# Performance work log

Hardware: AMD Instinct MI355X
Metric: run time of the kernel (lower is better)

## Reference

```python
import jax, jax.numpy as jnp
import numpy as np

D = 1024
N_HEADS = 16
HEAD_DIM = D // N_HEADS
EPS = 1e-09


def setup_inputs() -> dict:
    key = jax.random.key(0)
    ks = jax.random.split(key, 8)
    s = 0.02
    return {
        "x": jax.random.normal(ks[0], (2, 2048, D), jnp.float32),
        "Wq": jax.random.normal(ks[1], (D, D), jnp.float32) * s,
        "Wk": jax.random.normal(ks[2], (D, D), jnp.float32) * s,
        "Wv": jax.random.normal(ks[3], (D, D), jnp.float32) * s,
        "Wo": jax.random.normal(ks[4], (D, D), jnp.float32) * s,
        "W_up": jax.random.normal(ks[5], (4 * D, D), jnp.float32) * s,
        "W_down": jax.random.normal(ks[6], (D, 4 * D), jnp.float32) * s,
        "ln1_mean_scale": jnp.zeros((D,), jnp.float32),
        "ln1_std_scale": jnp.ones((D,), jnp.float32),
        "ln2_mean_scale": jnp.zeros((D,), jnp.float32),
        "ln2_std_scale": jnp.ones((D,), jnp.float32),
    }


def _ln(x, mean_scale, std_scale):
    mean = jnp.mean(x, axis=-1, keepdims=True)
    # torch .var() defaults to unbiased (ddof=1)
    std = jnp.sqrt(jnp.var(x, axis=-1, keepdims=True, ddof=1) + EPS)
    return (x - mean) / std * std_scale + mean_scale


def _attention(x, Wq, Wk, Wv, Wo):
    B, S, _ = x.shape
    # nn.Linear(bias=False): y = x @ W.T
    def heads(W):
        return (x @ W.T).reshape(B, S, N_HEADS, HEAD_DIM).transpose(0, 2, 1, 3)
    Q, K, V = heads(Wq), heads(Wk), heads(Wv)
    scale = jnp.sqrt(jnp.asarray(HEAD_DIM, Q.dtype))
    logits = jnp.einsum('bhqd,bhkd->bhqk', Q, K) / scale  # [B,H,S,S]
    causal = jnp.tril(jnp.ones((S, S), bool))
    logits = jnp.where(causal, logits, -jnp.inf)
    A = jax.nn.softmax(logits, axis=-1)
    preout = jnp.einsum('bhqk,bhkd->bhqd', A, V)  # [B,H,S,hd]
    # Wo.weight.T reshaped to (n_heads, d_head, d_model); per-head out then sum
    W_O = Wo.T.reshape(N_HEADS, HEAD_DIM, D)
    return jnp.einsum('bhsd,hdm->bsm', preout, W_O)


def _mlp(x, W_up, W_down):
    mid = jax.nn.gelu(x @ W_up.T, approximate=False)
    return mid @ W_down.T


def reference(x, Wq, Wk, Wv, Wo, W_up, W_down,
              ln1_mean_scale, ln1_std_scale, ln2_mean_scale, ln2_std_scale):
    x = x + _attention(_ln(x, ln1_mean_scale, ln1_std_scale), Wq, Wk, Wv, Wo)
    x = x + _mlp(_ln(x, ln2_mean_scale, ln2_std_scale), W_up, W_down)
    return x
```

## Files before the change

### kernel.cpp

```cpp
#include <hip/hip_runtime.h>
#include <hip/hip_bf16.h>
#include <cstdint>
#include <cstddef>

#define D_MODEL 1024
#define SEQ     2048
#define NTOK    4096
#define NH      16
#define HD      64

typedef __attribute__((ext_vector_type(8))) short sh8;
typedef __attribute__((ext_vector_type(4))) float f32x4;

#define GLL(g, s) __builtin_amdgcn_global_load_lds(                                   \
    (const __attribute__((address_space(1))) void*)(g),                               \
    (__attribute__((address_space(3))) void*)(s), 16, 0, 0)

__device__ __forceinline__ unsigned short f2b(float f) {
  union { float f; unsigned u; } v; v.f = f;
  unsigned r = v.u + 0x7FFFu + ((v.u >> 16) & 1u);
  return (unsigned short)(r >> 16);
}
__device__ __forceinline__ float b2f(unsigned short h) {
  union { unsigned u; float f; } v; v.u = ((unsigned)h) << 16;
  return v.f;
}

__global__ __launch_bounds__(256) void cast6_kernel(
    const float* __restrict__ q, const float* __restrict__ k, const float* __restrict__ v,
    const float* __restrict__ o, const float* __restrict__ u, const float* __restrict__ d,
    unsigned short* __restrict__ oq, unsigned short* __restrict__ ok,
    unsigned short* __restrict__ ov, unsigned short* __restrict__ oo,
    unsigned short* __restrict__ ou, unsigned short* __restrict__ od) {
  int bid = blockIdx.x;
  const float* src; unsigned short* dst; int base;
  if      (bid < 1024) { src = q; dst = oq; base = bid; }
  else if (bid < 2048) { src = k; dst = ok; base = bid - 1024; }
  else if (bid < 3072) { src = v; dst = ov; base = bid - 2048; }
  else if (bid < 4096) { src = o; dst = oo; base = bid - 3072; }
  else if (bid < 8192) { src = u; dst = ou; base = bid - 4096; }
  else                 { src = d; dst = od; base = bid - 8192; }
  int i = base * 1024 + threadIdx.x * 4;
  float4 vv = *(const float4*)(src + i);
  ushort4 w;
  w.x = f2b(vv.x); w.y = f2b(vv.y); w.z = f2b(vv.z); w.w = f2b(vv.w);
  *(ushort4*)(dst + i) = w;
}

__global__ __launch_bounds__(256) void ln_kernel(const float* __restrict__ x,
                                                 const float* __restrict__ msc,
                                                 const float* __restrict__ ssc,
                                                 unsigned short* __restrict__ out) {
  const int t = blockIdx.x;
  const int tid = threadIdx.x;
  const float4 v = ((const float4*)(x + (size_t)t * D_MODEL))[tid];
  float s = v.x + v.y + v.z + v.w;
  float q = v.x * v.x + v.y * v.y + v.z * v.z + v.w * v.w;
  #pragma unroll
  for (int off = 32; off; off >>= 1) {
    s += __shfl_xor(s, off);
    q += __shfl_xor(q, off);
  }
  __shared__ float sh[8];
  const int w = tid >> 6;
  if ((tid & 63) == 0) { sh[w * 2] = s; sh[w * 2 + 1] = q; }
  __syncthreads();
  s = sh[0] + sh[2] + sh[4] + sh[6];
  q = sh[1] + sh[3] + sh[5] + sh[7];
  const float mean = s * (1.0f / D_MODEL);
  const float var = (q - (float)D_MODEL * mean * mean) * (1.0f / (D_MODEL - 1));
  const float rstd = rsqrtf(var + 1e-9f);
  const float4 ms = ((const float4*)msc)[tid];
  const float4 ss = ((const float4*)ssc)[tid];
  ushort4 o;
  o.x = f2b((v.x - mean) * rstd * ss.x + ms.x);
  o.y = f2b((v.y - mean) * rstd * ss.y + ms.y);
  o.z = f2b((v.z - mean) * rstd * ss.z + ms.z);
  o.w = f2b((v.w - mean) * rstd * ss.w + ms.w);
  ((ushort4*)(out + (size_t)t * D_MODEL))[tid] = o;
}

template <bool WITH_X>
__global__ __launch_bounds__(256) void reduce2_kernel(const unsigned short* __restrict__ p0,
                                                      const unsigned short* __restrict__ p1,
                                                      const float* __restrict__ x,
                                                      float* __restrict__ out) {
  int i = (blockIdx.x * 256 + threadIdx.x) * 4;
  ushort4 a = *(const ushort4*)(p0 + i);
  ushort4 b = *(const ushort4*)(p1 + i);
  float4 base = WITH_X ? *(const float4*)(x + i) : *(const float4*)(out + i);
  float4 r;
  r.x = base.x + b2f(a.x) + b2f(b.x);
  r.y = base.y + b2f(a.y) + b2f(b.y);
  r.z = base.z + b2f(a.z) + b2f(b.z);
  r.w = base.w + b2f(a.w) + b2f(b.w);
  *(float4*)(out + i) = r;
}

__global__ __launch_bounds__(256) void vtrans_kernel(const unsigned short* __restrict__ qkv,
                                                     unsigned short* __restrict__ vt) {
  __shared__ unsigned short T[64][72];
  const int st = blockIdx.x;
  const int b  = blockIdx.y >> 4;
  const int dt = blockIdx.y & 15;
  const int tid = threadIdx.x;
  const int s0 = st * 64, d0 = dt * 64;
  const int r = tid >> 2, c0 = (tid & 3) * 16;
  const unsigned short* src = qkv + ((size_t)b * SEQ + s0 + r) * 3072 + 2 * D_MODEL + d0 + c0;
  *(uint4*)&T[r][c0]     = *(const uint4*)(src);
  *(uint4*)&T[r][c0 + 8] = *(const uint4*)(src + 8);
  __syncthreads();
  unsigned short buf[16] __attribute__((aligned(16)));
  #pragma unroll
  for (int j = 0; j < 16; j++) buf[j] = T[c0 + j][r];
  unsigned short* dst = vt + ((size_t)b * D_MODEL + d0 + r) * SEQ + s0 + c0;
  *(uint4*)(dst)     = *(uint4*)&buf[0];
  *(uint4*)(dst + 8) = *(uint4*)&buf[8];
}

template <int EP>
__global__ __launch_bounds__(256) void gemm_nt(const unsigned short* __restrict__ A,
                                               const unsigned short* __restrict__ B,
                                               int N, int LD, int Kext,
                                               unsigned short* __restrict__ Cbf,
                                               unsigned short* __restrict__ Cbf2) {
  __shared__ __align__(16) unsigned short As[128 * 64];
  __shared__ __align__(16) unsigned short Bs[128 * 64];
  const int tid = threadIdx.x;
  const int w = tid >> 6, l = tid & 63, ln = tid & 15, quad = (tid & 63) >> 4;
  const int wr = (w >> 1) * 64, wc = (w & 1) * 64;
  const int m0 = blockIdx.y * 128, n0 = blockIdx.x * 128;
  const int koff = blockIdx.z * Kext;

  const int sr = l >> 3, sc = l & 7;
  const unsigned short* AgS = A + (size_t)(m0 + w * 32 + sr) * LD + koff + ((sc ^ sr) * 8);
  const unsigned short* BgS = B + (size_t)(n0 + w * 32 + sr) * LD + koff + ((sc ^ sr) * 8);
  unsigned short* AsW = &As[(w * 32) * 64];
  unsigned short* BsW = &Bs[(w * 32) * 64];

  f32x4 acc[4][4] = {};

  for (int k0 = 0; k0 < Kext; k0 += 64) {
    __syncthreads();
    #pragma unroll
    for (int off = 0; off < 32; off += 8) {
      GLL(AgS + k0 + (size_t)off * LD, AsW + off * 64);
      GLL(BgS + k0 + (size_t)off * LD, BsW + off * 64);
    }
    __syncthreads();
    sh8 af[2][4], bfr[2][4];
    #pragma unroll
    for (int kk = 0; kk < 2; kk++) {
      #pragma unroll
      for (int i = 0; i < 4; i++)
        af[kk][i]  = *(const sh8*)&As[(wr + i * 16 + ln) * 64 + (((kk * 4 + quad) ^ (ln & 7)) * 8)];
      #pragma unroll
      for (int j = 0; j < 4; j++)
        bfr[kk][j] = *(const sh8*)&Bs[(wc + j * 16 + ln) * 64 + (((kk * 4 + quad) ^ (ln & 7)) * 8)];
    }
    #pragma unroll
    for (int kk = 0; kk < 2; kk++)
      #pragma unroll
      for (int i = 0; i < 4; i++)
        #pragma unroll
        for (int j = 0; j < 4; j++)
          acc[i][j] = __builtin_amdgcn_mfma_f32_16x16x32_bf16(af[kk][i], bfr[kk][j], acc[i][j], 0, 0, 0);
  }

  unsigned short* C = blockIdx.z ? Cbf2 : Cbf;
  #pragma unroll
  for (int i = 0; i < 4; i++) {
    #pragma unroll
    for (int rr = 0; rr < 4; rr++) {
      const int gm = m0 + wr + i * 16 + quad * 4 + rr;
      #pragma unroll
      for (int j = 0; j < 4; j++) {
        const int gn = n0 + wc + j * 16 + ln;
        const float v = acc[i][j][rr];
        const size_t idx = (size_t)gm * N + gn;
        if (EP == 0) {
          C[idx] = f2b(v);
        } else {
          const float g = 0.5f * v * (1.0f + erff(v * 0.70710678118654752f));
          C[idx] = f2b(g);
        }
      }
    }
  }
}

__global__ __launch_bounds__(256) void attn_kernel(const unsigned short* __restrict__ qkv,
                                                   const unsigned short* __restrict__ vt,
                                                   unsigned short* __restrict__ outp) {
  const int qt = (SEQ / 64 - 1) - blockIdx.x;
  const int bh = blockIdx.y;
  const int b = bh >> 4, h = bh & 15;
  const int tid = threadIdx.x;
  const int w = tid >> 6, l = tid & 63, ln = tid & 15, quad = (tid & 63) >> 4;
  const int q0 = qt * 64;

  __shared__ __align__(16) unsigned short Ks[64 * 64];
  __shared__ __align__(16) unsigned short Vs[64 * 64];
  __shared__ __align__(16) unsigned short Ps[4][16 * 72];

  const size_t rstride = 3 * D_MODEL;
  const unsigned short* Qg = qkv + (size_t)b * SEQ * rstride + h * HD;
  const unsigned short* Kg = Qg + D_MODEL;
  const unsigned short* Vg = vt + ((size_t)b * D_MODEL + h * HD) * SEQ;

  sh8 qf[2];
  {
    const unsigned short* qrow = Qg + (size_t)(q0 + w * 16 + ln) * rstride + quad * 8;
    qf[0] = *(const sh8*)(qrow);
    qf[1] = *(const sh8*)(qrow + 32);
  }

  const int lr3 = l >> 3, lp3 = l & 7;
  const int cS = (lp3 ^ lr3) * 8;
  const unsigned short* KgS = Kg + (size_t)(w * 16 + lr3) * rstride + cS;
  unsigned short* KsW = &Ks[(w * 16) * 64];
  const unsigned short* VgS = Vg + (size_t)(w * 16 + lr3) * SEQ + cS;
  unsigned short* VsW = &Vs[(w * 16) * 64];
  unsigned short* Psw = &Ps[w][0];

  f32x4 o[4] = {};
  float lpart[4] = {0.f, 0.f, 0.f, 0.f};
  const int rbase = q0 + w * 16 + quad * 4;

  auto tile = [&](int kt, bool diag) {
    __syncthreads();
    GLL(KgS + (size_t)(kt * 64) * rstride,     KsW);
    GLL(KgS + (size_t)(kt * 64 + 8) * rstride, KsW + 8 * 64);
    GLL(VgS + kt * 64,           VsW);
    GLL(VgS + 8 * SEQ + kt * 64, VsW + 8 * 64);
    __syncthreads();

    #pragma unroll
    for (int ct = 0; ct < 4; ct++) {
      const int k = ct * 16 + ln;
      f32x4 z = {};
      z = __builtin_amdgcn_mfma_f32_16x16x32_bf16(
          qf[0], *(const sh8*)&Ks[k * 64 + ((quad ^ (k & 7)) * 8)], z, 0, 0, 0);
      z = __builtin_amdgcn_mfma_f32_16x16x32_bf16(
          qf[1], *(const sh8*)&Ks[k * 64 + (((4 + quad) ^ (k & 7)) * 8)], z, 0, 0, 0);
      const int cg = kt * 64 + ct * 16 + ln;
      #pragma unroll
      for (int rr = 0; rr < 4; rr++) {
        float e = exp2f(fmaf(z[rr], 0.18033688011112042f, -5.770780163555853f));
        if (diag && cg > rbase + rr) e = 0.0f;
        lpart[rr] += e;
        Psw[(quad * 4 + rr) * 72 + ct * 16 + ln] = f2b(e);
      }
    }

    #pragma unroll
    for (int kk = 0; kk < 2; kk++) {
      sh8 pf = *(const sh8*)&Psw[ln * 72 + kk * 32 + quad * 8];
      #pragma unroll
      for (int c2 = 0; c2 < 4; c2++) {
        const int d = c2 * 16 + ln;
        sh8 vf = *(const sh8*)&Vs[d * 64 + ((((kk * 4 + quad) ^ (d & 7))) * 8)];
        o[c2] = __builtin_amdgcn_mfma_f32_16x16x32_bf16(pf, vf, o[c2], 0, 0, 0);
      }
    }
  };

  for (int kt = 0; kt < qt; kt++) tile(kt, false);
  tile(qt, true);

  #pragma unroll
  for (int rr = 0; rr < 4; rr++) {
    #pragma unroll
    for (int off = 1; off < 16; off <<= 1) lpart[rr] += __shfl_xor(lpart[rr], off);
  }

  #pragma unroll
  for (int rr = 0; rr < 4; rr++) {
    const int row = q0 + w * 16 + quad * 4 + rr;
    const float inv = 1.0f / lpart[rr];
    const size_t base = ((size_t)b * SEQ + row) * D_MODEL + h * HD;
    #pragma unroll
    for (int c2 = 0; c2 < 4; c2++)
      outp[base + c2 * 16 + ln] = f2b(o[c2][rr] * inv);
  }
}

extern "C" void kernel_launch(void* const* d_in, const int* in_sizes, int n_in,
                              void* d_out, int out_size, void* d_ws, size_t ws_size,
                              hipStream_t stream) {
  const float* x    = (const float*)d_in[0];
  const float* Wq   = (const float*)d_in[1];
  const float* Wk   = (const float*)d_in[2];
  const float* Wv   = (const float*)d_in[3];
  const float* Wo   = (const float*)d_in[4];
  const float* Wup  = (const float*)d_in[5];
  const float* Wdn  = (const float*)d_in[6];
  const float* ln1m = (const float*)d_in[7];
  const float* ln1s = (const float*)d_in[8];
  const float* ln2m = (const float*)d_in[9];
  const float* ln2s = (const float*)d_in[10];
  float* out = (float*)d_out;

  unsigned short* ws = (unsigned short*)d_ws;
  size_t off = 0;
  unsigned short* wqkv = ws + off; off += (size_t)3072 * 1024;
  unsigned short* wo   = ws + off; off += (size_t)1024 * 1024;
  unsigned short* wup  = ws + off; off += (size_t)4096 * 1024;
  unsigned short* wdn  = ws + off; off += (size_t)1024 * 4096;
  unsigned short* xln  = ws + off; off += (size_t)NTOK * 1024;
  unsigned short* qkvb = ws + off; off += (size_t)NTOK * 3072;
  unsigned short* pre  = ws + off; off += (size_t)NTOK * 1024;
  unsigned short* mid  = qkvb;
  unsigned short* vtg  = xln;
  unsigned short* po0  = qkvb;
  unsigned short* po1  = qkvb + (size_t)NTOK * 1024;
  unsigned short* pd0  = ws;
  unsigned short* pd1  = xln;

  cast6_kernel<<<12288, 256, 0, stream>>>(Wq, Wk, Wv, Wo, Wup, Wdn,
      wqkv, wqkv + (size_t)1024 * 1024, wqkv + (size_t)2 * 1024 * 1024, wo, wup, wdn);

  ln_kernel<<<NTOK, 256, 0, stream>>>(x, ln1m, ln1s, xln);
  gemm_nt<0><<<dim3(24, 32, 1), 256, 0, stream>>>(xln, wqkv, 3072, 1024, 1024, qkvb, nullptr);
  vtrans_kernel<<<dim3(32, 32), 256, 0, stream>>>(qkvb, vtg);
  attn_kernel<<<dim3(SEQ / 64, 2 * NH), 256, 0, stream>>>(qkvb, vtg, pre);
  gemm_nt<0><<<dim3(8, 32, 2), 256, 0, stream>>>(pre, wo, 1024, 1024, 512, po0, po1);
  reduce2_kernel<true><<<4096, 256, 0, stream>>>(po0, po1, x, out);
  ln_kernel<<<NTOK, 256, 0, stream>>>(out, ln2m, ln2s, xln);
  gemm_nt<2><<<dim3(32, 32, 1), 256, 0, stream>>>(xln, wup, 4096, 1024, 1024, mid, nullptr);
  gemm_nt<0><<<dim3(8, 32, 2), 256, 0, stream>>>(mid, wdn, 1024, 4096, 2048, pd0, pd1);
  reduce2_kernel<false><<<4096, 256, 0, stream>>>(pd0, pd1, nullptr, out);
}
```

Baseline: 373.3 us.

## Split attention key range across two blocks and combine partial outputs

The causal attention kernel now launches two blocks per query tile. Each block handles alternating key tiles and writes unnormalized bf16 partial outputs plus partial row sums. A new combine kernel adds the two partials and divides by the summed denominators. This doubles the grid and shortens the longest per-block causal loop, which should improve load balance and occupancy. The cost is an extra kernel launch, extra partial-output traffic, and bf16 rounding of unnormalized values, using the output buffer and the dead QKV weight region as scratch.

```diff
diff --git a/kernel.cpp b/kernel.cpp
--- a/kernel.cpp
+++ b/kernel.cpp
@@ -97,6 +97,24 @@
   *(float4*)(out + i) = r;
 }
 
+__global__ __launch_bounds__(256) void attn_combine_kernel(
+    unsigned short* __restrict__ p0, const unsigned short* __restrict__ p1,
+    const float* __restrict__ l0, const float* __restrict__ l1) {
+  int i = (blockIdx.x * 256 + threadIdx.x) * 4;
+  const int tok = i >> 10, ch = i & 1023;
+  const int b = tok >> 11, s = tok & 2047, h = ch >> 6;
+  const int lidx = ((b << 4) + h) * 2048 + s;
+  const float inv = 1.0f / (l0[lidx] + l1[lidx]);
+  ushort4 a = *(const ushort4*)(p0 + i);
+  ushort4 c = *(const ushort4*)(p1 + i);
+  ushort4 r;
+  r.x = f2b((b2f(a.x) + b2f(c.x)) * inv);
+  r.y = f2b((b2f(a.y) + b2f(c.y)) * inv);
+  r.z = f2b((b2f(a.z) + b2f(c.z)) * inv);
+  r.w = f2b((b2f(a.w) + b2f(c.w)) * inv);
+  *(ushort4*)(p0 + i) = r;
+}
+
 __global__ __launch_bounds__(256) void vtrans_kernel(const unsigned short* __restrict__ qkv,
                                                      unsigned short* __restrict__ vt) {
   __shared__ unsigned short T[64][72];
@@ -191,8 +209,12 @@
 
 __global__ __launch_bounds__(256) void attn_kernel(const unsigned short* __restrict__ qkv,
                                                    const unsigned short* __restrict__ vt,
-                                                   unsigned short* __restrict__ outp) {
+                                                   unsigned short* __restrict__ p0,
+                                                   unsigned short* __restrict__ p1,
+                                                   float* __restrict__ l0,
+                                                   float* __restrict__ l1) {
   const int qt = (SEQ / 64 - 1) - blockIdx.x;
+  const int z  = blockIdx.z;
   const int bh = blockIdx.y;
   const int b = bh >> 4, h = bh & 15;
   const int tid = threadIdx.x;
@@ -238,15 +260,15 @@
     #pragma unroll
     for (int ct = 0; ct < 4; ct++) {
       const int k = ct * 16 + ln;
-      f32x4 z = {};
-      z = __builtin_amdgcn_mfma_f32_16x16x32_bf16(
-          qf[0], *(const sh8*)&Ks[k * 64 + ((quad ^ (k & 7)) * 8)], z, 0, 0, 0);
-      z = __builtin_amdgcn_mfma_f32_16x16x32_bf16(
-          qf[1], *(const sh8*)&Ks[k * 64 + (((4 + quad) ^ (k & 7)) * 8)], z, 0, 0, 0);
+      f32x4 zz = {};
+      zz = __builtin_amdgcn_mfma_f32_16x16x32_bf16(
+          qf[0], *(const sh8*)&Ks[k * 64 + ((quad ^ (k & 7)) * 8)], zz, 0, 0, 0);
+      zz = __builtin_amdgcn_mfma_f32_16x16x32_bf16(
+          qf[1], *(const sh8*)&Ks[k * 64 + (((4 + quad) ^ (k & 7)) * 8)], zz, 0, 0, 0);
       const int cg = kt * 64 + ct * 16 + ln;
       #pragma unroll
       for (int rr = 0; rr < 4; rr++) {
-        float e = exp2f(fmaf(z[rr], 0.18033688011112042f, -5.770780163555853f));
+        float e = exp2f(fmaf(zz[rr], 0.18033688011112042f, -5.770780163555853f));
         if (diag && cg > rbase + rr) e = 0.0f;
         lpart[rr] += e;
         Psw[(quad * 4 + rr) * 72 + ct * 16 + ln] = f2b(e);
@@ -265,8 +287,8 @@
     }
   };
 
-  for (int kt = 0; kt < qt; kt++) tile(kt, false);
-  tile(qt, true);
+  for (int kt = z; kt < qt; kt += 2) tile(kt, false);
+  if ((qt & 1) == z) tile(qt, true);
 
   #pragma unroll
   for (int rr = 0; rr < 4; rr++) {
@@ -274,14 +296,20 @@
     for (int off = 1; off < 16; off <<= 1) lpart[rr] += __shfl_xor(lpart[rr], off);
   }
 
+  unsigned short* P = z ? p1 : p0;
+  float* L = z ? l1 : l0;
+  if (ln == 0) {
+    #pragma unroll
+    for (int rr = 0; rr < 4; rr++)
+      L[((size_t)bh << 11) + q0 + w * 16 + quad * 4 + rr] = lpart[rr];
+  }
   #pragma unroll
   for (int rr = 0; rr < 4; rr++) {
     const int row = q0 + w * 16 + quad * 4 + rr;
-    const float inv = 1.0f / lpart[rr];
     const size_t base = ((size_t)b * SEQ + row) * D_MODEL + h * HD;
     #pragma unroll
     for (int c2 = 0; c2 < 4; c2++)
-      outp[base + c2 * 16 + ln] = f2b(o[c2][rr] * inv);
+      P[base + c2 * 16 + ln] = f2b(o[c2][rr]);
   }
 }
 
@@ -316,6 +344,9 @@
   unsigned short* po1  = qkvb + (size_t)NTOK * 1024;
   unsigned short* pd0  = ws;
   unsigned short* pd1  = xln;
+  unsigned short* ap1  = (unsigned short*)out;
+  float* al0 = (float*)wqkv;
+  float* al1 = al0 + (size_t)2 * NH * SEQ;
 
   cast6_kernel<<<12288, 256, 0, stream>>>(Wq, Wk, Wv, Wo, Wup, Wdn,
       wqkv, wqkv + (size_t)1024 * 1024, wqkv + (size_t)2 * 1024 * 1024, wo, wup, wdn);
@@ -323,7 +354,8 @@
   ln_kernel<<<NTOK, 256, 0, stream>>>(x, ln1m, ln1s, xln);
   gemm_nt<0><<<dim3(24, 32, 1), 256, 0, stream>>>(xln, wqkv, 3072, 1024, 1024, qkvb, nullptr);
   vtrans_kernel<<<dim3(32, 32), 256, 0, stream>>>(qkvb, vtg);
-  attn_kernel<<<dim3(SEQ / 64, 2 * NH), 256, 0, stream>>>(qkvb, vtg, pre);
+  attn_kernel<<<dim3(SEQ / 64, 2 * NH, 2), 256, 0, stream>>>(qkvb, vtg, pre, ap1, al0, al1);
+  attn_combine_kernel<<<4096, 256, 0, stream>>>(pre, ap1, al0, al1);
   gemm_nt<0><<<dim3(8, 32, 2), 256, 0, stream>>>(pre, wo, 1024, 1024, 512, po0, po1);
   reduce2_kernel<true><<<4096, 256, 0, stream>>>(po0, po1, x, out);
   ln_kernel<<<NTOK, 256, 0, stream>>>(out, ln2m, ln2s, xln);
```

Result: no change. 373.9 us (+0.2%).

## Load attention K/V fragments directly from global per wave, drop shared tiles

Applied to the files above, without the earlier changes.

The attention kernel no longer stages K and V tiles in shared memory with block-wide barriers. Each wave now handles its own 16-row query strip, reads its K and V MFMA fragments straight from global memory, and walks only as many key tiles as its causal range needs. This removes the __syncthreads and LDS traffic and lets waves finish on their own, at the cost of loading K/V once per wave instead of once per block. That multiplies global and L2 traffic and exposes load latency with no overlap.

```diff
diff --git a/kernel.cpp b/kernel.cpp
--- a/kernel.cpp
+++ b/kernel.cpp
@@ -192,16 +192,14 @@
 __global__ __launch_bounds__(256) void attn_kernel(const unsigned short* __restrict__ qkv,
                                                    const unsigned short* __restrict__ vt,
                                                    unsigned short* __restrict__ outp) {
-  const int qt = (SEQ / 64 - 1) - blockIdx.x;
+  const int tid = threadIdx.x;
+  const int w = tid >> 6, ln = tid & 15, quad = (tid & 63) >> 4;
+  const int strip = 127 - (blockIdx.x * 4 + w);
   const int bh = blockIdx.y;
   const int b = bh >> 4, h = bh & 15;
-  const int tid = threadIdx.x;
-  const int w = tid >> 6, l = tid & 63, ln = tid & 15, quad = (tid & 63) >> 4;
-  const int q0 = qt * 64;
-
-  __shared__ __align__(16) unsigned short Ks[64 * 64];
-  __shared__ __align__(16) unsigned short Vs[64 * 64];
+
   __shared__ __align__(16) unsigned short Ps[4][16 * 72];
+  unsigned short* Psw = &Ps[w][0];
 
   const size_t rstride = 3 * D_MODEL;
   const unsigned short* Qg = qkv + (size_t)b * SEQ * rstride + h * HD;
@@ -210,43 +208,41 @@
 
   sh8 qf[2];
   {
-    const unsigned short* qrow = Qg + (size_t)(q0 + w * 16 + ln) * rstride + quad * 8;
+    const unsigned short* qrow = Qg + (size_t)(strip * 16 + ln) * rstride + quad * 8;
     qf[0] = *(const sh8*)(qrow);
     qf[1] = *(const sh8*)(qrow + 32);
   }
 
-  const int lr3 = l >> 3, lp3 = l & 7;
-  const int cS = (lp3 ^ lr3) * 8;
-  const unsigned short* KgS = Kg + (size_t)(w * 16 + lr3) * rstride + cS;
-  unsigned short* KsW = &Ks[(w * 16) * 64];
-  const unsigned short* VgS = Vg + (size_t)(w * 16 + lr3) * SEQ + cS;
-  unsigned short* VsW = &Vs[(w * 16) * 64];
-  unsigned short* Psw = &Ps[w][0];
-
   f32x4 o[4] = {};
   float lpart[4] = {0.f, 0.f, 0.f, 0.f};
-  const int rbase = q0 + w * 16 + quad * 4;
-
-  auto tile = [&](int kt, bool diag) {
-    __syncthreads();
-    GLL(KgS + (size_t)(kt * 64) * rstride,     KsW);
-    GLL(KgS + (size_t)(kt * 64 + 8) * rstride, KsW + 8 * 64);
-    GLL(VgS + kt * 64,           VsW);
-    GLL(VgS + 8 * SEQ + kt * 64, VsW + 8 * 64);
-    __syncthreads();
-
+  const int rbase = strip * 16 + quad * 4;
+  const int nkt = (strip >> 2) + 1;
+
+  for (int kt = 0; kt < nkt; kt++) {
+    const bool diag = (kt == nkt - 1);
+    sh8 kf[4][2], vf[4][2];
+    const unsigned short* kbase = Kg + (size_t)(kt * 64 + ln) * rstride + quad * 8;
     #pragma unroll
     for (int ct = 0; ct < 4; ct++) {
-      const int k = ct * 16 + ln;
-      f32x4 z = {};
-      z = __builtin_amdgcn_mfma_f32_16x16x32_bf16(
-          qf[0], *(const sh8*)&Ks[k * 64 + ((quad ^ (k & 7)) * 8)], z, 0, 0, 0);
-      z = __builtin_amdgcn_mfma_f32_16x16x32_bf16(
-          qf[1], *(const sh8*)&Ks[k * 64 + (((4 + quad) ^ (k & 7)) * 8)], z, 0, 0, 0);
+      kf[ct][0] = *(const sh8*)(kbase + (size_t)(ct * 16) * rstride);
+      kf[ct][1] = *(const sh8*)(kbase + (size_t)(ct * 16) * rstride + 32);
+    }
+    const unsigned short* vbase = Vg + (size_t)ln * SEQ + kt * 64 + quad * 8;
+    #pragma unroll
+    for (int c2 = 0; c2 < 4; c2++) {
+      vf[c2][0] = *(const sh8*)(vbase + (size_t)(c2 * 16) * SEQ);
+      vf[c2][1] = *(const sh8*)(vbase + (size_t)(c2 * 16) * SEQ + 32);
+    }
+
+    #pragma unroll
+    for (int ct = 0; ct < 4; ct++) {
+      f32x4 zz = {};
+      zz = __builtin_amdgcn_mfma_f32_16x16x32_bf16(qf[0], kf[ct][0], zz, 0, 0, 0);
+      zz = __builtin_amdgcn_mfma_f32_16x16x32_bf16(qf[1], kf[ct][1], zz, 0, 0, 0);
       const int cg = kt * 64 + ct * 16 + ln;
       #pragma unroll
       for (int rr = 0; rr < 4; rr++) {
-        float e = exp2f(fmaf(z[rr], 0.18033688011112042f, -5.770780163555853f));
+        float e = exp2f(fmaf(zz[rr], 0.18033688011112042f, -5.770780163555853f));
         if (diag && cg > rbase + rr) e = 0.0f;
         lpart[rr] += e;
         Psw[(quad * 4 + rr) * 72 + ct * 16 + ln] = f2b(e);
@@ -257,26 +253,19 @@
     for (int kk = 0; kk < 2; kk++) {
       sh8 pf = *(const sh8*)&Psw[ln * 72 + kk * 32 + quad * 8];
       #pragma unroll
-      for (int c2 = 0; c2 < 4; c2++) {
-        const int d = c2 * 16 + ln;
-        sh8 vf = *(const sh8*)&Vs[d * 64 + ((((kk * 4 + quad) ^ (d & 7))) * 8)];
-        o[c2] = __builtin_amdgcn_mfma_f32_16x16x32_bf16(pf, vf, o[c2], 0, 0, 0);
-      }
-    }
-  };
-
-  for (int kt = 0; kt < qt; kt++) tile(kt, false);
-  tile(qt, true);
+      for (int c2 = 0; c2 < 4; c2++)
+        o[c2] = __builtin_amdgcn_mfma_f32_16x16x32_bf16(pf, vf[c2][kk], o[c2], 0, 0, 0);
+    }
+  }
 
   #pragma unroll
   for (int rr = 0; rr < 4; rr++) {
     #pragma unroll
     for (int off = 1; off < 16; off <<= 1) lpart[rr] += __shfl_xor(lpart[rr], off);
   }
-
   #pragma unroll
   for (int rr = 0; rr < 4; rr++) {
-    const int row = q0 + w * 16 + quad * 4 + rr;
+    const int row = strip * 16 + quad * 4 + rr;
     const float inv = 1.0f / lpart[rr];
     const size_t base = ((size_t)b * SEQ + row) * D_MODEL + h * HD;
     #pragma unroll
@@ -323,7 +312,7 @@
   ln_kernel<<<NTOK, 256, 0, stream>>>(x, ln1m, ln1s, xln);
   gemm_nt<0><<<dim3(24, 32, 1), 256, 0, stream>>>(xln, wqkv, 3072, 1024, 1024, qkvb, nullptr);
   vtrans_kernel<<<dim3(32, 32), 256, 0, stream>>>(qkvb, vtg);
-  attn_kernel<<<dim3(SEQ / 64, 2 * NH), 256, 0, stream>>>(qkvb, vtg, pre);
+  attn_kernel<<<dim3(32, 2 * NH), 256, 0, stream>>>(qkvb, vtg, pre);
   gemm_nt<0><<<dim3(8, 32, 2), 256, 0, stream>>>(pre, wo, 1024, 1024, 512, po0, po1);
   reduce2_kernel<true><<<4096, 256, 0, stream>>>(po0, po1, x, out);
   ln_kernel<<<NTOK, 256, 0, stream>>>(out, ln2m, ln2s, xln);
```

Result: slower. 583.5 us (+56.3%).
